# Kernel optimization log

Hardware: AMD Instinct MI355X
Metric: run time of the kernel (lower is better)

## Reference

```python
import jax, jax.numpy as jnp
import numpy as np

B, N, D, H, L = 2, 1024, 256, 4, 9
HEAD = D // H  # 64
IMG_H, IMG_W = 480, 640
SINKHORN_ITERS = 20
CH = [3, 32, 64, 128, 256]


def setup_inputs() -> dict:
    key = jax.random.key(0)
    ks = iter(jax.random.split(key, 80))
    def rn(shape, s):
        return jax.random.normal(next(ks), shape, dtype=jnp.float32) * s
    inp = {}
    size = jnp.array([IMG_W, IMG_H], jnp.float32)
    inp['kpts0'] = jax.random.uniform(next(ks), (B, N, 2), dtype=jnp.float32) * size
    inp['kpts1'] = jax.random.uniform(next(ks), (B, N, 2), dtype=jnp.float32) * size
    inp['scores0'] = jax.random.uniform(next(ks), (B, N), dtype=jnp.float32)
    inp['scores1'] = jax.random.uniform(next(ks), (B, N), dtype=jnp.float32)
    inp['desc0'] = rn((B, D, N), 1.0)
    inp['desc1'] = rn((B, D, N), 1.0)
    for i in range(4):
        inp['kenc_w%d' % i] = rn((CH[i + 1], CH[i]), CH[i] ** -0.5)
        inp['kenc_b%d' % i] = rn((CH[i + 1],), 0.02)
        if i < 3:
            inp['kenc_g%d' % i] = jnp.ones((CH[i + 1],), jnp.float32)
            inp['kenc_be%d' % i] = jnp.zeros((CH[i + 1],), jnp.float32)
    s = D ** -0.5
    inp['gnn_proj_w'] = rn((L, 3, D, D), s)
    inp['gnn_proj_b'] = rn((L, 3, D), 0.02)
    inp['gnn_merge_w'] = rn((L, D, D), s)
    inp['gnn_merge_b'] = rn((L, D), 0.02)
    inp['gnn_mlp1_w'] = rn((L, 2 * D, 2 * D), (2 * D) ** -0.5)
    inp['gnn_mlp1_b'] = rn((L, 2 * D), 0.02)
    inp['gnn_ln_g'] = jnp.ones((L, 2 * D), jnp.float32)
    inp['gnn_ln_b'] = jnp.zeros((L, 2 * D), jnp.float32)
    inp['gnn_mlp2_w'] = rn((L, D, 2 * D), (2 * D) ** -0.5)
    inp['gnn_mlp2_b'] = jnp.zeros((L, D), jnp.float32)
    inp['final_w'] = rn((D, D), s)
    inp['final_b'] = rn((D,), 0.02)
    inp['bin_score'] = jnp.array(1.0, jnp.float32)
    return inp


def _conv1(x, w, b):
    # 1x1 Conv1d == per-position matmul: x [B,C,N], w [O,C], b [O]
    return jnp.einsum('oc,bcn->bon', w, x) + b[None, :, None]


def _layernorm(x, g, b, eps=1e-6):
    # matches source LayerNorm: normalize over channel dim (-2), std with ddof=1, eps added to std
    mean = jnp.mean(x, axis=1, keepdims=True)
    std = jnp.std(x, axis=1, keepdims=True, ddof=1)
    return g[None, :, None] * (x - mean) / (std + eps) + b[None, :, None]


def _normalize_kpts(kpts):
    size = jnp.array([IMG_W, IMG_H], jnp.float32)
    center = size / 2.0
    scaling = jnp.max(size) * 0.7
    return (kpts - center) / scaling


def _attn(x, src, pw, pb, mw, mb):
    # pw [3,D,D]; view(B, head_dim, n_heads, N) matches torch .view on [B,D,N]
    q = _conv1(x, pw[0], pb[0]).reshape(B, HEAD, H, -1)
    k = _conv1(src, pw[1], pb[1]).reshape(B, HEAD, H, -1)
    v = _conv1(src, pw[2], pb[2]).reshape(B, HEAD, H, -1)
    scores = jnp.einsum('bdhn,bdhm->bhnm', q, k) / (HEAD ** 0.5)
    prob = jax.nn.softmax(scores, axis=-1)
    msg = jnp.einsum('bhnm,bdhm->bdhn', prob, v).reshape(B, D, -1)
    return _conv1(msg, mw, mb)


def _sinkhorn(Z, log_mu, log_nu, iters):
    def step(uv, _):
        u, v = uv
        u = log_mu - jax.scipy.special.logsumexp(Z + v[:, None, :], axis=2)
        v = log_nu - jax.scipy.special.logsumexp(Z + u[:, :, None], axis=1)
        return (u, v), None
    init = (jnp.zeros_like(log_mu), jnp.zeros_like(log_nu))
    (u, v), _ = jax.lax.scan(step, init, None, length=iters)
    return Z + u[:, :, None] + v[:, None, :]


def _log_ot(scores, alpha, iters):
    b, m, n = scores.shape
    bins0 = jnp.broadcast_to(alpha, (b, m, 1))
    bins1 = jnp.broadcast_to(alpha, (b, 1, n))
    a = jnp.broadcast_to(alpha, (b, 1, 1))
    couplings = jnp.concatenate([jnp.concatenate([scores, bins0], -1),
                                 jnp.concatenate([bins1, a], -1)], 1)
    norm = jnp.asarray(-np.log(float(m + n)), jnp.float32)
    log_mu = jnp.concatenate([jnp.full((m,), norm, jnp.float32),
                              jnp.array([np.log(float(n))], jnp.float32) + norm])
    log_nu = jnp.concatenate([jnp.full((n,), norm, jnp.float32),
                              jnp.array([np.log(float(m))], jnp.float32) + norm])
    log_mu = jnp.broadcast_to(log_mu, (b, m + 1))
    log_nu = jnp.broadcast_to(log_nu, (b, n + 1))
    Z = _sinkhorn(couplings, log_mu, log_nu, iters)
    return Z - norm


def _superglue_fwd(kpts0, kpts1, scores0, scores1, desc0, desc1,
                   kenc_w0, kenc_b0, kenc_g0, kenc_be0,
                   kenc_w1, kenc_b1, kenc_g1, kenc_be1,
                   kenc_w2, kenc_b2, kenc_g2, kenc_be2,
                   kenc_w3, kenc_b3,
                   gnn_proj_w, gnn_proj_b, gnn_merge_w, gnn_merge_b,
                   gnn_mlp1_w, gnn_mlp1_b, gnn_ln_g, gnn_ln_b,
                   gnn_mlp2_w, gnn_mlp2_b, final_w, final_b, bin_score):
    kenc = [(kenc_w0, kenc_b0, kenc_g0, kenc_be0),
            (kenc_w1, kenc_b1, kenc_g1, kenc_be1),
            (kenc_w2, kenc_b2, kenc_g2, kenc_be2),
            (kenc_w3, kenc_b3, None, None)]

    def encode(kpts, sc):
        x = jnp.concatenate([_normalize_kpts(kpts).transpose(0, 2, 1), sc[:, None, :]], 1)  # [B,3,N]
        for (w, b, g, be) in kenc:
            x = _conv1(x, w, b)
            if g is not None:
                x = jax.nn.relu(_layernorm(x, g, be))
        return x

    desc0 = desc0 + encode(kpts0, scores0)
    desc1 = desc1 + encode(kpts1, scores1)

    # only 'cross' GNN layers execute in this fork ('self' layers are skipped via continue)
    for i in range(L):
        def prop(x, src):
            msg = _attn(x, src, gnn_proj_w[i], gnn_proj_b[i], gnn_merge_w[i], gnn_merge_b[i])
            y = jnp.concatenate([x, msg], 1)  # [B,2D,N]
            y = jax.nn.relu(_layernorm(_conv1(y, gnn_mlp1_w[i], gnn_mlp1_b[i]), gnn_ln_g[i], gnn_ln_b[i]))
            return _conv1(y, gnn_mlp2_w[i], gnn_mlp2_b[i])
        d0 = prop(desc0, desc1)
        d1 = prop(desc1, desc0)
        desc0, desc1 = desc0 + d0, desc1 + d1

    mdesc0 = _conv1(desc0, final_w, final_b)
    mdesc1 = _conv1(desc1, final_w, final_b)
    sc = jnp.einsum('bdn,bdm->bnm', mdesc0, mdesc1) / (D ** 0.5)
    return _log_ot(sc, bin_score, SINKHORN_ITERS)  # [B, N+1, N+1] log assignment matrix


def reference(kpts0, kpts1, scores0, scores1, desc0, desc1,
              kenc_w0, kenc_b0, kenc_g0, kenc_be0,
              kenc_w1, kenc_b1, kenc_g1, kenc_be1,
              kenc_w2, kenc_b2, kenc_g2, kenc_be2,
              kenc_w3, kenc_b3,
              gnn_proj_w, gnn_proj_b, gnn_merge_w, gnn_merge_b,
              gnn_mlp1_w, gnn_mlp1_b, gnn_ln_g, gnn_ln_b,
              gnn_mlp2_w, gnn_mlp2_b, final_w, final_b, bin_score):
    return _superglue_fwd(kpts0, kpts1, scores0, scores1, desc0, desc1,
                          kenc_w0, kenc_b0, kenc_g0, kenc_be0,
                          kenc_w1, kenc_b1, kenc_g1, kenc_be1,
                          kenc_w2, kenc_b2, kenc_g2, kenc_be2,
                          kenc_w3, kenc_b3,
                          gnn_proj_w, gnn_proj_b, gnn_merge_w, gnn_merge_b,
                          gnn_mlp1_w, gnn_mlp1_b, gnn_ln_g, gnn_ln_b,
                          gnn_mlp2_w, gnn_mlp2_b, final_w, final_b, bin_score)
```

## Files before the change

### kernel.cpp

```cpp
#include <hip/hip_runtime.h>
#include <hip/hip_bf16.h>
#include <math.h>

#define DEVI static __device__ __forceinline__

namespace {
constexpr int Bc   = 2;
constexpr int Nc   = 1024;
constexpr int Dc   = 256;
constexpr int NP1c = 1025;
constexpr int LDZ  = 1028;
constexpr int LDV  = 1028;
constexpr float LN_EPS = 1e-6f;
constexpr float NORMV  = -7.6246189861593985f;
constexpr float LOGNV  =  6.9314718055994531f;
}

typedef __attribute__((ext_vector_type(8))) short bf16x8;
typedef __attribute__((ext_vector_type(4))) float f32x4;

DEVI void split2(float v, __hip_bfloat16& h, __hip_bfloat16& l) {
    h = __float2bfloat16(v);
    l = __float2bfloat16(v - __bfloat162float(h));
}

#define GLDS16(gp, lp) __builtin_amdgcn_global_load_lds( \
    (const __attribute__((address_space(1))) void*)(gp), \
    (__attribute__((address_space(3))) void*)(lp), 16, 0, 0)

DEVI float block_sum_256(float v, float* scratch) {
    int t = threadIdx.x;
    scratch[t] = v;
    __syncthreads();
    for (int s = 128; s > 0; s >>= 1) {
        if (t < s) scratch[t] += scratch[t + s];
        __syncthreads();
    }
    float r = scratch[0];
    __syncthreads();
    return r;
}

DEVI void ln_relu_inplace(float* x, const float* g, const float* be, int C, float* scratch) {
    int t = threadIdx.x;
    float v = (t < C) ? x[t] : 0.f;
    float mean = block_sum_256(v, scratch) / (float)C;
    float dv = (t < C) ? (x[t] - mean) : 0.f;
    float var = block_sum_256(dv * dv, scratch) / (float)(C - 1);
    float rstd = 1.f / (sqrtf(var) + LN_EPS);
    if (t < C) x[t] = fmaxf(g[t] * dv * rstd + be[t], 0.f);
    __syncthreads();
}

__global__ __launch_bounds__(256) void kenc_kernel(
    const float* __restrict__ kpts, const float* __restrict__ scr,
    const float* __restrict__ desc_in, float* __restrict__ desc_out,
    __hip_bfloat16* __restrict__ catHi, __hip_bfloat16* __restrict__ catLo,
    const float* __restrict__ w0, const float* __restrict__ b0,
    const float* __restrict__ g0, const float* __restrict__ be0,
    const float* __restrict__ w1T, const float* __restrict__ b1,
    const float* __restrict__ g1, const float* __restrict__ be1,
    const float* __restrict__ w2T, const float* __restrict__ b2,
    const float* __restrict__ g2, const float* __restrict__ be2,
    const float* __restrict__ w3T, const float* __restrict__ b3)
{
    __shared__ float xa[256], xb[256], scratch[256];
    const int n = blockIdx.x, b = blockIdx.y, t = threadIdx.x;
    if (t == 0) {
        float kx = kpts[((long)b * Nc + n) * 2 + 0];
        float ky = kpts[((long)b * Nc + n) * 2 + 1];
        xa[0] = (kx - 320.f) * (1.f / 448.f);
        xa[1] = (ky - 240.f) * (1.f / 448.f);
        xa[2] = scr[b * Nc + n];
    }
    __syncthreads();
    if (t < 32) { float a = b0[t]; for (int c = 0; c < 3;  ++c) a += w0[t*3 + c] * xa[c]; xb[t] = a; }
    __syncthreads();
    ln_relu_inplace(xb, g0, be0, 32, scratch);
    if (t < 64) {
        float a = b1[t];
        #pragma unroll 8
        for (int c = 0; c < 32;  ++c) a += w1T[c*64 + t] * xb[c];
        xa[t] = a;
    }
    __syncthreads();
    ln_relu_inplace(xa, g1, be1, 64, scratch);
    if (t < 128) {
        float a = b2[t];
        #pragma unroll 8
        for (int c = 0; c < 64;  ++c) a += w2T[c*128 + t] * xa[c];
        xb[t] = a;
    }
    __syncthreads();
    ln_relu_inplace(xb, g2, be2, 128, scratch);
    {   float a = b3[t];
        #pragma unroll 8
        for (int c = 0; c < 128; ++c) a += w3T[c*256 + t] * xb[c];
        float v = desc_in[((long)b * Dc + t) * Nc + n] + a;
        desc_out[((long)b * Nc + n) * Dc + t] = v;
        __hip_bfloat16 h, l; split2(v, h, l);
        long cr = ((long)b * Nc + n) * 512 + t;
        catHi[cr] = h; catLo[cr] = l;
    }
}

__global__ __launch_bounds__(256) void transposeW(
    const float* __restrict__ src, float* __restrict__ dst, int O, int C)
{
    long i = (long)blockIdx.x * 256 + threadIdx.x;
    if (i >= (long)O * C) return;
    int o = (int)(i / C), c = (int)(i % C);
    dst[(long)c * O + o] = src[i];
}

template<int BM, int BN, int EPI, int BLO, int ALO>
__global__ __launch_bounds__(256) void mfma_nt(
    const short* __restrict__ Ahi0, const short* __restrict__ Alo0, int lda,
    const short* __restrict__ Bhi0, const short* __restrict__ Blo0, int ldb,
    int K, float scale, const float* __restrict__ bias,
    float* __restrict__ outF, __hip_bfloat16* __restrict__ outHi,
    __hip_bfloat16* __restrict__ outLo,
    __hip_bfloat16* __restrict__ outHi2, __hip_bfloat16* __restrict__ outHi3,
    int ldo,
    long aS1, long bS1, long oS1)
{
    constexpr int MI = BM / 32;
    constexpr int NI = BN / 32;
    constexpr int instA = BM / 16, instB = BN / 16;
    constexpr int OFF_AH = 0;
    constexpr int OFF_AL = BM * 32;
    constexpr int OFF_BH = (1 + ALO) * BM * 32;
    constexpr int OFF_BL = OFF_BH + BN * 32;
    constexpr int CHUNK = ((1 + ALO) * BM + (1 + BLO) * BN) * 32;
    __shared__ short smem[2 * CHUNK];

    const int z = blockIdx.z;
    const long aOff = z * aS1, bOff = z * bS1, oOff = z * oS1;
    const short* Ah = Ahi0 + aOff;
    const short* Al = ALO ? (Alo0 + aOff) : nullptr;
    const short* Bh = Bhi0 + bOff;
    const short* Bl = BLO ? (Blo0 + bOff) : nullptr;

    const int m0 = blockIdx.y * BM, n0 = blockIdx.x * BN;
    const int t = threadIdx.x, lane = t & 63, wid = t >> 6;
    const int lr = lane & 15, lg = lane >> 4;
    const int wr = wid >> 1, wc = wid & 1;

    f32x4 acc[MI][NI];
    for (int mi = 0; mi < MI; ++mi)
        for (int ni = 0; ni < NI; ++ni)
            acc[mi][ni] = f32x4{0.f, 0.f, 0.f, 0.f};

    for (int k0 = 0; k0 < K; k0 += 64) {
        constexpr int total = (1 + ALO) * instA + (1 + BLO) * instB;
        for (int q = wid; q < total; q += 4) {
            const short* gsrc; int ldg, mi, ploff, row0;
            if (q < instA)                      { gsrc = Ah; ldg = lda; mi = q;          ploff = OFF_AH; row0 = m0; }
            else if (ALO && q < 2 * instA)      { gsrc = Al; ldg = lda; mi = q - instA;  ploff = OFF_AL; row0 = m0; }
            else {
                int rb = q - (1 + ALO) * instA;
                if (rb < instB) { gsrc = Bh; mi = rb;         ploff = OFF_BH; }
                else            { gsrc = Bl; mi = rb - instB; ploff = OFF_BL; }
                ldg = ldb; row0 = n0;
            }
            const short* g = gsrc + (long)(row0 + mi * 16 + lr) * ldg + (k0 + lg * 8);
            GLDS16(g,      smem + ploff + mi * 512);
            GLDS16(g + 32, smem + CHUNK + ploff + mi * 512);
        }
        __syncthreads();
        #pragma unroll
        for (int kc2 = 0; kc2 < 2; ++kc2) {
            const short* sm2 = smem + kc2 * CHUNK;
            bf16x8 ah[MI], al[MI];
            #pragma unroll
            for (int mi = 0; mi < MI; ++mi) {
                ah[mi] = *(const bf16x8*)(sm2 + OFF_AH + ((wr * MI + mi) * 64 + lane) * 8);
                if (ALO) al[mi] = *(const bf16x8*)(sm2 + OFF_AL + ((wr * MI + mi) * 64 + lane) * 8);
            }
            #pragma unroll
            for (int ni = 0; ni < NI; ++ni) {
                bf16x8 bh = *(const bf16x8*)(sm2 + OFF_BH + ((wc * NI + ni) * 64 + lane) * 8);
                #pragma unroll
                for (int mi = 0; mi < MI; ++mi) {
                    acc[mi][ni] = __builtin_amdgcn_mfma_f32_16x16x32_bf16(ah[mi], bh, acc[mi][ni], 0, 0, 0);
                    if (ALO) acc[mi][ni] = __builtin_amdgcn_mfma_f32_16x16x32_bf16(al[mi], bh, acc[mi][ni], 0, 0, 0);
                }
                if (BLO) {
                    bf16x8 bl = *(const bf16x8*)(sm2 + OFF_BL + ((wc * NI + ni) * 64 + lane) * 8);
                    #pragma unroll
                    for (int mi = 0; mi < MI; ++mi)
                        acc[mi][ni] = __builtin_amdgcn_mfma_f32_16x16x32_bf16(ah[mi], bl, acc[mi][ni], 0, 0, 0);
                }
            }
        }
        __syncthreads();
    }

    for (int mi = 0; mi < MI; ++mi) {
        for (int i = 0; i < 4; ++i) {
            int row = m0 + wr * (BM / 2) + mi * 16 + lg * 4 + i;
            for (int ni = 0; ni < NI; ++ni) {
                int col = n0 + wc * (BN / 2) + ni * 16 + lr;
                float v = acc[mi][ni][i] * scale;
                if (bias) v += bias[col];
                if (EPI == 0) {
                    outF[(long)row * ldo + col + oOff] = v;
                } else if (EPI == 1) {
                    __hip_bfloat16 h, l;
                    split2(v, h, l);
                    outHi[(long)row * ldo + col + oOff] = h;
                    outLo[(long)row * ldo + col + oOff] = l;
                } else if (EPI == 2) {
                    int dirb = row >> 10, rloc = row & 1023;
                    int tq = col >> 8, within = col & 255;
                    int h4 = within >> 6, hd = within & 63;
                    __hip_bfloat16 hh = __float2bfloat16(v);
                    if (tq == 2) {
                        int w2 = rloc >> 8, mloc = rloc & 255;
                        int lane2 = ((mloc & 31) >> 3) * 16 + (hd & 15);
                        long idx = ((((long)(dirb*4+h4)*4 + w2)*8 + (mloc>>5))*4 + (hd>>4))*512 + lane2*8 + (mloc&7);
                        outHi2[idx] = hh;
                    } else {
                        int lane2 = ((hd & 31) >> 3) * 16 + (rloc & 15);
                        long idx = (((long)(dirb*4+h4)*64 + (rloc>>4))*2 + (hd>>5))*512 + lane2*8 + (hd&7);
                        if (tq == 0) outHi[idx] = hh;
                        else         outHi3[idx] = hh;
                    }
                } else {
                    long i256 = (long)row * 256 + col;
                    v += outF[i256];
                    outF[i256] = v;
                    __hip_bfloat16 h, l;
                    split2(v, h, l);
                    outHi[(long)row * 512 + col] = h;
                    outLo[(long)row * 512 + col] = l;
                }
            }
        }
    }
}

__global__ __launch_bounds__(256) void attn_fused(
    const __hip_bfloat16* __restrict__ qFh,
    const __hip_bfloat16* __restrict__ kFh, const __hip_bfloat16* __restrict__ vFh,
    __hip_bfloat16* __restrict__ catHi)
{
    __shared__ short pLds[4 * 16 * 256];
    __shared__ float redm[4][16], reds[4][16];
    const int y = blockIdx.y;
    const int dir = y >> 3, b = (y >> 2) & 1, h = y & 3;
    const int q0 = blockIdx.x * 16;
    const int t = threadIdx.x, lane = t & 63, w = t >> 6;
    const int lr = lane & 15, lg = lane >> 4;
    const int dbQ = dir * 2 + b;
    const int srcdb = (1 - dir) * 2 + b;
    const short* qh = (const short*)qFh;
    const short* kh = (const short*)kFh;
    const short* vh = (const short*)vFh;

    const long qbase = (((long)(dbQ * 4 + h)) * 64 + (q0 >> 4)) * 2;
    bf16x8 ah[2];
    #pragma unroll
    for (int kc = 0; kc < 2; ++kc)
        ah[kc] = *(const bf16x8*)(qh + (qbase + kc) * 512 + lane * 8);

    f32x4 acc[16];
    #pragma unroll
    for (int ni = 0; ni < 16; ++ni) acc[ni] = f32x4{0.f, 0.f, 0.f, 0.f};

    const long kbase0 = (((long)(srcdb * 4 + h)) * 64 + w * 16) * 2;
    #pragma unroll
    for (int ni = 0; ni < 16; ++ni) {
        long kb = (kbase0 + ni * 2) * 512 + lane * 8;
        bf16x8 bh0 = *(const bf16x8*)(kh + kb);
        bf16x8 bh1 = *(const bf16x8*)(kh + kb + 512);
        acc[ni] = __builtin_amdgcn_mfma_f32_16x16x32_bf16(ah[0], bh0, acc[ni], 0, 0, 0);
        acc[ni] = __builtin_amdgcn_mfma_f32_16x16x32_bf16(ah[1], bh1, acc[ni], 0, 0, 0);
    }

    float mx[4] = {-1e30f, -1e30f, -1e30f, -1e30f};
    #pragma unroll
    for (int ni = 0; ni < 16; ++ni)
        #pragma unroll
        for (int i = 0; i < 4; ++i) {
            float v = acc[ni][i] * 0.125f;
            acc[ni][i] = v;
            mx[i] = fmaxf(mx[i], v);
        }
    #pragma unroll
    for (int off = 1; off < 16; off <<= 1)
        #pragma unroll
        for (int i = 0; i < 4; ++i) mx[i] = fmaxf(mx[i], __shfl_xor(mx[i], off));
    if (lr == 0)
        #pragma unroll
        for (int i = 0; i < 4; ++i) redm[w][lg * 4 + i] = mx[i];
    __syncthreads();
    float Mv[4];
    #pragma unroll
    for (int i = 0; i < 4; ++i)
        Mv[i] = fmaxf(fmaxf(redm[0][lg*4+i], redm[1][lg*4+i]),
                      fmaxf(redm[2][lg*4+i], redm[3][lg*4+i]));
    float sm[4] = {0.f, 0.f, 0.f, 0.f};
    #pragma unroll
    for (int ni = 0; ni < 16; ++ni)
        #pragma unroll
        for (int i = 0; i < 4; ++i) {
            float e = __expf(acc[ni][i] - Mv[i]);
            acc[ni][i] = e;
            sm[i] += e;
        }
    #pragma unroll
    for (int off = 1; off < 16; off <<= 1)
        #pragma unroll
        for (int i = 0; i < 4; ++i) sm[i] += __shfl_xor(sm[i], off);
    if (lr == 0)
        #pragma unroll
        for (int i = 0; i < 4; ++i) reds[w][lg * 4 + i] = sm[i];
    __syncthreads();
    float inv[4];
    #pragma unroll
    for (int i = 0; i < 4; ++i)
        inv[i] = 1.f / (reds[0][lg*4+i] + reds[1][lg*4+i] + reds[2][lg*4+i] + reds[3][lg*4+i]);

    char* pB = (char*)pLds + w * 8192;
    #pragma unroll
    for (int ni = 0; ni < 16; ++ni)
        #pragma unroll
        for (int i = 0; i < 4; ++i) {
            int q = lg * 4 + i, m = ni * 16 + lr;
            int byte = (q * 512 + m * 2) ^ ((q & 7) << 4);
            *(short*)(pB + byte) = (short)__bfloat16_as_ushort(__float2bfloat16(acc[ni][i] * inv[i]));
        }
    __syncthreads();

    f32x4 acc2[4];
    #pragma unroll
    for (int bi = 0; bi < 4; ++bi) acc2[bi] = f32x4{0.f, 0.f, 0.f, 0.f};
    const long vbase0 = (((long)(srcdb * 4 + h)) * 4 + w) * 8;
    #pragma unroll
    for (int km = 0; km < 8; ++km) {
        int rb = (lr * 512 + km * 64 + lg * 16) ^ ((lr & 7) << 4);
        bf16x8 pa = *(const bf16x8*)(pB + rb);
        #pragma unroll
        for (int bi = 0; bi < 4; ++bi) {
            long vr = ((vbase0 + km) * 4 + bi) * 512 + lane * 8;
            bf16x8 vhf = *(const bf16x8*)(vh + vr);
            acc2[bi] = __builtin_amdgcn_mfma_f32_16x16x32_bf16(pa, vhf, acc2[bi], 0, 0, 0);
        }
    }
    __syncthreads();
    float* pr = (float*)pLds;
    #pragma unroll
    for (int bi = 0; bi < 4; ++bi)
        #pragma unroll
        for (int i = 0; i < 4; ++i)
            pr[w * 1024 + (lg * 4 + i) * 64 + bi * 16 + lr] = acc2[bi][i];
    __syncthreads();
    #pragma unroll
    for (int k = 0; k < 4; ++k) {
        int e = t + k * 256;
        float v = pr[e] + pr[1024 + e] + pr[2048 + e] + pr[3072 + e];
        int q = e >> 6, d = e & 63;
        long a = ((long)dbQ * 1024 + q0 + q) * 512 + 256 + h * 64 + d;
        catHi[a] = __float2bfloat16(v);
    }
}

__global__ __launch_bounds__(256) void ln_relu_w(
    const float* __restrict__ y, const float* __restrict__ g, const float* __restrict__ be,
    __hip_bfloat16* __restrict__ hi)
{
    const int t = threadIdx.x, lane = t & 63, w = t >> 6;
    const long row = (long)blockIdx.x * 4 + w;
    const float* src = y + row * 512;
    float4 v0 = ((const float4*)src)[lane * 2];
    float4 v1 = ((const float4*)src)[lane * 2 + 1];
    float s = v0.x + v0.y + v0.z + v0.w + v1.x + v1.y + v1.z + v1.w;
    float q = v0.x*v0.x + v0.y*v0.y + v0.z*v0.z + v0.w*v0.w
            + v1.x*v1.x + v1.y*v1.y + v1.z*v1.z + v1.w*v1.w;
    #pragma unroll
    for (int off = 1; off < 64; off <<= 1) {
        s += __shfl_xor(s, off);
        q += __shfl_xor(q, off);
    }
    float mean = s / 512.f;
    float var = fmaxf((q - 512.f * mean * mean) / 511.f, 0.f);
    float rstd = 1.f / (sqrtf(var) + LN_EPS);
    float4 g0 = ((const float4*)g)[lane * 2], g1 = ((const float4*)g)[lane * 2 + 1];
    float4 b0 = ((const float4*)be)[lane * 2], b1 = ((const float4*)be)[lane * 2 + 1];
    float xv[8] = {v0.x, v0.y, v0.z, v0.w, v1.x, v1.y, v1.z, v1.w};
    float gv[8] = {g0.x, g0.y, g0.z, g0.w, g1.x, g1.y, g1.z, g1.w};
    float bv[8] = {b0.x, b0.y, b0.z, b0.w, b1.x, b1.y, b1.z, b1.w};
    bf16x8 outv;
    #pragma unroll
    for (int k = 0; k < 8; ++k) {
        float o = fmaxf(gv[k] * (xv[k] - mean) * rstd + bv[k], 0.f);
        outv[k] = (short)__bfloat16_as_ushort(__float2bfloat16(o));
    }
    *(bf16x8*)((short*)hi + row * 512 + lane * 8) = outv;
}

__global__ __launch_bounds__(256) void wconv_plain(
    const float* __restrict__ w, __hip_bfloat16* __restrict__ hi, __hip_bfloat16* __restrict__ lo, long total)
{
    long i = (long)blockIdx.x * 256 + threadIdx.x;
    if (i >= total) return;
    __hip_bfloat16 h, l; split2(w[i], h, l);
    hi[i] = h; lo[i] = l;
}

__global__ __launch_bounds__(256) void wconv_proj(
    const float* __restrict__ w, __hip_bfloat16* __restrict__ hi, __hip_bfloat16* __restrict__ lo)
{
    long i = (long)blockIdx.x * 256 + threadIdx.x;
    if (i >= 9L * 768 * 256) return;
    long l9 = i / (768 * 256);
    int rem = (int)(i % (768 * 256));
    int op = rem / 256, c = rem % 256;
    int tq = op / 256, within = op % 256;
    int h = within / 64, hd = within % 64;
    int o = tq * 256 + hd * 4 + h;
    float v = w[(l9 * 768 + o) * 256 + c];
    __hip_bfloat16 hh, ll; split2(v, hh, ll);
    hi[i] = hh; lo[i] = ll;
}

__global__ void wconv_proj_bias(const float* __restrict__ b, float* __restrict__ bp)
{
    int i = blockIdx.x * 256 + threadIdx.x;
    if (i >= 9 * 768) return;
    int l9 = i / 768, op = i % 768;
    int tq = op / 256, within = op % 256;
    int h = within / 64, hd = within % 64;
    bp[i] = b[(l9 * 3 + tq) * 256 + hd * 4 + h];
}

__global__ __launch_bounds__(256) void wconv_mergeT(
    const float* __restrict__ w, __hip_bfloat16* __restrict__ hi, __hip_bfloat16* __restrict__ lo)
{
    long i = (long)blockIdx.x * 256 + threadIdx.x;
    if (i >= 9L * 256 * 256) return;
    long l9 = i / (256 * 256);
    int rem = (int)(i % (256 * 256));
    int c = rem / 256, j = rem % 256;
    int h = c / 64, hd = c % 64;
    float v = w[(l9 * 256 + j) * 256 + (hd * 4 + h)];
    __hip_bfloat16 hh, ll; split2(v, hh, ll);
    hi[i] = hh; lo[i] = ll;
}

__global__ __launch_bounds__(256) void wconv_m1(
    const float* __restrict__ w,
    __hip_bfloat16* __restrict__ m1cHi, __hip_bfloat16* __restrict__ m1cLo,
    __hip_bfloat16* __restrict__ m1bHi, __hip_bfloat16* __restrict__ m1bLo)
{
    long i = (long)blockIdx.x * 256 + threadIdx.x;
    if (i >= 9L * 512 * 512) return;
    long lo9 = i / 512;
    int c = (int)(i % 512);
    __hip_bfloat16 hh, ll; split2(w[i], hh, ll);
    if (c < 256) { m1cHi[lo9 * 512 + c] = hh; m1cLo[lo9 * 512 + c] = ll; }
    else         { m1bHi[lo9 * 256 + c - 256] = hh; m1bLo[lo9 * 256 + c - 256] = ll; }
}

__global__ __launch_bounds__(64) void bias_fold(
    const float* __restrict__ w1, const float* __restrict__ b1,
    const float* __restrict__ bm, float* __restrict__ out)
{
    int og = blockIdx.x;
    int l = og >> 9, o = og & 511;
    int t = threadIdx.x;
    float s = 0.f;
    for (int j = t; j < 256; j += 64)
        s += w1[((long)l * 512 + o) * 512 + 256 + j] * bm[l * 256 + j];
    for (int off = 32; off > 0; off >>= 1) s += __shfl_down(s, off);
    if (t == 0) out[og] = b1[(long)l * 512 + o] + s;
}

__global__ void bins_fill(float* __restrict__ Z, const float* __restrict__ alpha_p)
{
    float alpha = alpha_p[0];
    int idx = blockIdx.x * 256 + threadIdx.x;
    int b = blockIdx.y;
    float* Zb = Z + (long)b * NP1c * LDZ;
    if (idx < NP1c) Zb[(long)1024 * LDZ + idx] = alpha;
    else { int i = idx - NP1c; if (i < 1024) Zb[(long)i * LDZ + 1024] = alpha; }
}

__global__ void transpose_np1(const float* __restrict__ Z, float* __restrict__ ZT)
{
    __shared__ float tile[32][33];
    int b = blockIdx.z;
    int i0 = blockIdx.y * 32, j0 = blockIdx.x * 32;
    int tx = threadIdx.x, ty = threadIdx.y;
    const float* Zb = Z + (long)b * NP1c * LDZ;
    float* Tb = ZT + (long)b * NP1c * LDZ;
    for (int ii = ty; ii < 32; ii += 8) {
        int i = i0 + ii, j = j0 + tx;
        if (i < NP1c && j < NP1c) tile[ii][tx] = Zb[(long)i * LDZ + j];
    }
    __syncthreads();
    for (int jj = ty; jj < 32; jj += 8) {
        int j = j0 + jj, i = i0 + tx;
        if (j < NP1c && i < NP1c) Tb[(long)j * LDZ + i] = tile[tx][jj];
    }
}

__global__ void zero_vec(float* __restrict__ v, int n)
{
    int i = blockIdx.x * 256 + threadIdx.x;
    if (i < n) v[i] = 0.f;
}

__global__ __launch_bounds__(256) void sinkhorn_lse(
    const float* __restrict__ M, const float* __restrict__ addv, float* __restrict__ outv)
{
    const int t = threadIdx.x, lane = t & 63, w = t >> 6;
    long rowid = (long)blockIdx.x * 4 + w;
    if (rowid >= 2 * NP1c) return;
    int b = rowid >= NP1c ? 1 : 0;
    int i = (int)(rowid - (long)b * NP1c);
    const float* row = M + ((long)b * NP1c + i) * LDZ;
    const float* av = addv + (long)b * LDV;
    float m = -1e30f, s = 0.f;
    #pragma unroll
    for (int k = 0; k < 4; ++k) {
        float4 x = ((const float4*)row)[lane * 4 + k];
        float4 a = ((const float4*)av)[lane * 4 + k];
        float u0 = x.x + a.x, u1 = x.y + a.y, u2 = x.z + a.z, u3 = x.w + a.w;
        float mk = fmaxf(fmaxf(u0, u1), fmaxf(u2, u3));
        float sk = __expf(u0 - mk) + __expf(u1 - mk) + __expf(u2 - mk) + __expf(u3 - mk);
        if (mk > m) { s = s * __expf(m - mk) + sk; m = mk; }
        else        { s += sk * __expf(mk - m); }
    }
    if (lane == 0) {
        float v4 = row[1024] + av[1024];
        if (v4 > m) { s = s * __expf(m - v4) + 1.f; m = v4; }
        else        { s += __expf(v4 - m); }
    }
    #pragma unroll
    for (int off = 1; off < 64; off <<= 1) {
        float m2 = __shfl_xor(m, off);
        float s2 = __shfl_xor(s, off);
        float mm = fmaxf(m, m2);
        s = s * __expf(m - mm) + s2 * __expf(m2 - mm);
        m = mm;
    }
    if (lane == 0) {
        float lse = m + __logf(s);
        float lmu = (i < 1024) ? NORMV : (LOGNV + NORMV);
        outv[(long)b * LDV + i] = lmu - lse;
    }
}

__global__ __launch_bounds__(256) void final_out_k(
    const float* __restrict__ Z, const float* __restrict__ u,
    const float* __restrict__ v, float* __restrict__ outp)
{
    const int i = blockIdx.x, b = blockIdx.y, t = threadIdx.x;
    const float* row = Z + ((long)b * NP1c + i) * LDZ;
    float* orow = outp + ((long)b * NP1c + i) * NP1c;
    float ui = u[(long)b * LDV + i];
    for (int j = t; j < NP1c; j += 256)
        orow[j] = row[j] + ui + v[(long)b * LDV + j] - NORMV;
}

extern "C" void kernel_launch(void* const* d_in, const int* in_sizes, int n_in,
                              void* d_out, int out_size, void* d_ws, size_t ws_size,
                              hipStream_t stream)
{
    (void)in_sizes; (void)n_in; (void)out_size; (void)ws_size;
    const float* kpts0   = (const float*)d_in[0];
    const float* kpts1   = (const float*)d_in[1];
    const float* scores0 = (const float*)d_in[2];
    const float* scores1 = (const float*)d_in[3];
    const float* desc0   = (const float*)d_in[4];
    const float* desc1   = (const float*)d_in[5];
    const float* kw0 = (const float*)d_in[6];  const float* kb0 = (const float*)d_in[7];
    const float* kg0 = (const float*)d_in[8];  const float* ke0 = (const float*)d_in[9];
    const float* kw1 = (const float*)d_in[10]; const float* kb1 = (const float*)d_in[11];
    const float* kg1 = (const float*)d_in[12]; const float* ke1 = (const float*)d_in[13];
    const float* kw2 = (const float*)d_in[14]; const float* kb2 = (const float*)d_in[15];
    const float* kg2 = (const float*)d_in[16]; const float* ke2 = (const float*)d_in[17];
    const float* kw3 = (const float*)d_in[18]; const float* kb3 = (const float*)d_in[19];
    const float* gnn_proj_w  = (const float*)d_in[20];
    const float* gnn_proj_b  = (const float*)d_in[21];
    const float* gnn_merge_w = (const float*)d_in[22];
    const float* gnn_merge_b = (const float*)d_in[23];
    const float* gnn_mlp1_w  = (const float*)d_in[24];
    const float* gnn_mlp1_b  = (const float*)d_in[25];
    const float* gnn_ln_g    = (const float*)d_in[26];
    const float* gnn_ln_b    = (const float*)d_in[27];
    const float* gnn_mlp2_w  = (const float*)d_in[28];
    const float* gnn_mlp2_b  = (const float*)d_in[29];
    const float* final_w     = (const float*)d_in[30];
    const float* final_b     = (const float*)d_in[31];
    const float* bin_score   = (const float*)d_in[32];

    char* wsb = (char*)d_ws;
    size_t off = 0;
    auto alloc = [&](size_t bytes) -> void* {
        void* p = wsb + off;
        off = (off + bytes + 255) & ~(size_t)255;
        return p;
    };
    typedef __hip_bfloat16 bf;
    const long ROWS = 4L * Nc;
    float* descF  = (float*)alloc(ROWS * 256 * 4);
    float* ybufF  = (float*)alloc(ROWS * 512 * 4);
    float* Zm     = (float*)alloc((long)Bc * NP1c * LDZ * 4);
    float* ZT     = (float*)alloc((long)Bc * NP1c * LDZ * 4);
    float* uvec   = (float*)alloc(Bc * LDV * 4);
    float* vvec   = (float*)alloc(Bc * LDV * 4);
    float* projBp = (float*)alloc(9L * 768 * 4);
    float* b1c    = (float*)alloc(9L * 512 * 4);
    float* kw1T   = (float*)alloc(32L * 64 * 4);
    float* kw2T   = (float*)alloc(64L * 128 * 4);
    float* kw3T   = (float*)alloc(128L * 256 * 4);
    bf* catHi = (bf*)alloc(ROWS * 512 * 2);  bf* catLo = (bf*)alloc(ROWS * 512 * 2);
    bf* qFh = (bf*)alloc(1048576 * 2);
    bf* kFh = (bf*)alloc(1048576 * 2);
    bf* vFh = (bf*)alloc(1048576 * 2);
    bf* ybHi  = (bf*)alloc(ROWS * 512 * 2);
    bf* mdHi  = (bf*)alloc(ROWS * 256 * 2);  bf* mdLo  = (bf*)alloc(ROWS * 256 * 2);
    bf* projHi = (bf*)alloc(9L*768*256*2);   bf* projLo = (bf*)alloc(9L*768*256*2);
    bf* mrgTHi = (bf*)alloc(9L*256*256*2);   bf* mrgTLo = (bf*)alloc(9L*256*256*2);
    bf* m1bHi  = (bf*)alloc(9L*512*256*2);   bf* m1bLo  = (bf*)alloc(9L*512*256*2);
    bf* m1cHi  = (bf*)alloc(9L*512*512*2);   bf* m1cLo  = (bf*)alloc(9L*512*512*2);
    bf* m2Hi   = (bf*)alloc(9L*256*512*2);   bf* m2Lo   = (bf*)alloc(9L*256*512*2);
    bf* finHi  = (bf*)alloc(256L*256*2);     bf* finLo  = (bf*)alloc(256L*256*2);

    wconv_proj<<<dim3((9*768*256+255)/256), 256, 0, stream>>>(gnn_proj_w, projHi, projLo);
    wconv_proj_bias<<<dim3(27), 256, 0, stream>>>(gnn_proj_b, projBp);
    wconv_mergeT<<<dim3((9*256*256+255)/256), 256, 0, stream>>>(gnn_merge_w, mrgTHi, mrgTLo);
    wconv_m1<<<dim3((int)((9L*512*512+255)/256)), 256, 0, stream>>>(gnn_mlp1_w, m1cHi, m1cLo, m1bHi, m1bLo);
    wconv_plain<<<dim3((9*256*512+255)/256), 256, 0, stream>>>(gnn_mlp2_w, m2Hi, m2Lo, 9L*256*512);
    wconv_plain<<<dim3((256*256+255)/256), 256, 0, stream>>>(final_w, finHi, finLo, 256L*256);
    bias_fold<<<dim3(9*512), 64, 0, stream>>>(gnn_mlp1_w, gnn_mlp1_b, gnn_merge_b, b1c);
    transposeW<<<dim3((64*32+255)/256), 256, 0, stream>>>(kw1, kw1T, 64, 32);
    transposeW<<<dim3((128*64+255)/256), 256, 0, stream>>>(kw2, kw2T, 128, 64);
    transposeW<<<dim3((256*128+255)/256), 256, 0, stream>>>(kw3, kw3T, 256, 128);
    mfma_nt<128,128,1,1,1><<<dim3(2,4,9), 256, 0, stream>>>(
        (const short*)m1bHi, (const short*)m1bLo, 256,
        (const short*)mrgTHi, (const short*)mrgTLo, 256,
        256, 1.f, nullptr,
        nullptr, m1cHi + 256, m1cLo + 256, nullptr, nullptr, 512,
        512L*256, 256L*256, 512L*512);

    kenc_kernel<<<dim3(Nc, Bc), 256, 0, stream>>>(kpts0, scores0, desc0, descF,
        catHi, catLo,
        kw0, kb0, kg0, ke0, kw1T, kb1, kg1, ke1, kw2T, kb2, kg2, ke2, kw3T, kb3);
    kenc_kernel<<<dim3(Nc, Bc), 256, 0, stream>>>(kpts1, scores1, desc1, descF + 2L*Nc*256,
        catHi + 2L*Nc*512, catLo + 2L*Nc*512,
        kw0, kb0, kg0, ke0, kw1T, kb1, kg1, ke1, kw2T, kb2, kg2, ke2, kw3T, kb3);

    for (int l = 0; l < 9; ++l) {
        mfma_nt<64,64,2,0,0><<<dim3(12,64,1), 256, 0, stream>>>(
            (const short*)catHi, nullptr, 512,
            (const short*)(projHi + (long)l*768*256), nullptr, 256,
            256, 1.f, projBp + (long)l*768,
            nullptr, qFh, nullptr, vFh, kFh, 0,
            0, 0, 0);
        attn_fused<<<dim3(64, 16), 256, 0, stream>>>(qFh, kFh, vFh, catHi);
        mfma_nt<64,64,0,0,0><<<dim3(8,64,1), 256, 0, stream>>>(
            (const short*)catHi, nullptr, 512,
            (const short*)(m1cHi + (long)l*512*512), nullptr, 512,
            512, 1.f, b1c + (long)l*512,
            ybufF, nullptr, nullptr, nullptr, nullptr, 512,
            0, 0, 0);
        ln_relu_w<<<dim3(1024), 256, 0, stream>>>(
            ybufF, gnn_ln_g + (long)l*512, gnn_ln_b + (long)l*512, ybHi);
        mfma_nt<64,64,3,0,0><<<dim3(4,64,1), 256, 0, stream>>>(
            (const short*)ybHi, nullptr, 512,
            (const short*)(m2Hi + (long)l*256*512), nullptr, 512,
            512, 1.f, gnn_mlp2_b + (long)l*256,
            descF, catHi, catLo, nullptr, nullptr, 0,
            0, 0, 0);
    }

    mfma_nt<64,64,1,0,1><<<dim3(4,64,1), 256, 0, stream>>>(
        (const short*)catHi, (const short*)catLo, 512,
        (const short*)finHi, nullptr, 256,
        256, 1.f, final_b,
        nullptr, mdHi, mdLo, nullptr, nullptr, 256,
        0, 0, 0);
    mfma_nt<64,64,0,1,1><<<dim3(16,16,2), 256, 0, stream>>>(
        (const short*)mdHi, (const short*)mdLo, 256,
        (const short*)mdHi + 2048L*256, (const short*)mdLo + 2048L*256, 256,
        256, 1.f/16.f, nullptr,
        Zm, nullptr, nullptr, nullptr, nullptr, LDZ,
        1024L*256, 1024L*256, (long)NP1c*LDZ);
    bins_fill<<<dim3(9,2), 256, 0, stream>>>(Zm, bin_score);

    transpose_np1<<<dim3(33,33,2), dim3(32,8), 0, stream>>>(Zm, ZT);
    zero_vec<<<dim3((2*LDV+255)/256), 256, 0, stream>>>(vvec, Bc * LDV);
    zero_vec<<<dim3((2*LDV+255)/256), 256, 0, stream>>>(uvec, Bc * LDV);
    for (int it = 0; it < 20; ++it) {
        sinkhorn_lse<<<dim3(513), 256, 0, stream>>>(Zm, vvec, uvec);
        sinkhorn_lse<<<dim3(513), 256, 0, stream>>>(ZT, uvec, vvec);
    }
    final_out_k<<<dim3(NP1c, Bc), 256, 0, stream>>>(Zm, uvec, vvec, (float*)d_out);
}
```

Measured before the change: 907.4 us.

## Merge kenc launches, write MLP1 output as bf16, deepen GEMM K-chunk

Merges the two keypoint-encoder launches into one grid and the two zero-fill launches into one, cutting launch count. The MLP1 GEMM now writes a bf16 intermediate in place of fp32, and LayerNorm reads and overwrites that bf16 buffer, halving that round-trip traffic and dropping the fp32 scratch buffer. The GEMM template gains a K-chunk count parameter, set to 4 for most GEMMs, so each sync stage loads 128 K elements, at the cost of more LDS per block. Rounding the pre-LayerNorm activations to bf16 adds some numerical error.

```diff
diff --git a/kernel.cpp b/kernel.cpp
--- a/kernel.cpp
+++ b/kernel.cpp
@@ -24,6 +24,8 @@
     l = __float2bfloat16(v - __bfloat162float(h));
 }
 
+DEVI float bf2f(short u) { return __uint_as_float(((unsigned)(unsigned short)u) << 16); }
+
 #define GLDS16(gp, lp) __builtin_amdgcn_global_load_lds( \
     (const __attribute__((address_space(1))) void*)(gp), \
     (__attribute__((address_space(3))) void*)(lp), 16, 0, 0)
@@ -53,8 +55,10 @@
 }
 
 __global__ __launch_bounds__(256) void kenc_kernel(
-    const float* __restrict__ kpts, const float* __restrict__ scr,
-    const float* __restrict__ desc_in, float* __restrict__ desc_out,
+    const float* __restrict__ kpts0, const float* __restrict__ kpts1,
+    const float* __restrict__ scr0, const float* __restrict__ scr1,
+    const float* __restrict__ desc0, const float* __restrict__ desc1,
+    float* __restrict__ descF,
     __hip_bfloat16* __restrict__ catHi, __hip_bfloat16* __restrict__ catLo,
     const float* __restrict__ w0, const float* __restrict__ b0,
     const float* __restrict__ g0, const float* __restrict__ be0,
@@ -65,7 +69,11 @@
     const float* __restrict__ w3T, const float* __restrict__ b3)
 {
     __shared__ float xa[256], xb[256], scratch[256];
-    const int n = blockIdx.x, b = blockIdx.y, t = threadIdx.x;
+    const int n = blockIdx.x, db = blockIdx.y, t = threadIdx.x;
+    const int dir = db >> 1, b = db & 1;
+    const float* kpts = dir ? kpts1 : kpts0;
+    const float* scr  = dir ? scr1  : scr0;
+    const float* dsc  = dir ? desc1 : desc0;
     if (t == 0) {
         float kx = kpts[((long)b * Nc + n) * 2 + 0];
         float ky = kpts[((long)b * Nc + n) * 2 + 1];
@@ -96,10 +104,10 @@
     {   float a = b3[t];
         #pragma unroll 8
         for (int c = 0; c < 128; ++c) a += w3T[c*256 + t] * xb[c];
-        float v = desc_in[((long)b * Dc + t) * Nc + n] + a;
-        desc_out[((long)b * Nc + n) * Dc + t] = v;
+        float v = dsc[((long)b * Dc + t) * Nc + n] + a;
+        descF[((long)db * Nc + n) * Dc + t] = v;
         __hip_bfloat16 h, l; split2(v, h, l);
-        long cr = ((long)b * Nc + n) * 512 + t;
+        long cr = ((long)db * Nc + n) * 512 + t;
         catHi[cr] = h; catLo[cr] = l;
     }
 }
@@ -113,7 +121,7 @@
     dst[(long)c * O + o] = src[i];
 }
 
-template<int BM, int BN, int EPI, int BLO, int ALO>
+template<int BM, int BN, int EPI, int BLO, int ALO, int BKC>
 __global__ __launch_bounds__(256) void mfma_nt(
     const short* __restrict__ Ahi0, const short* __restrict__ Alo0, int lda,
     const short* __restrict__ Bhi0, const short* __restrict__ Blo0, int ldb,
@@ -132,7 +140,7 @@
     constexpr int OFF_BH = (1 + ALO) * BM * 32;
     constexpr int OFF_BL = OFF_BH + BN * 32;
     constexpr int CHUNK = ((1 + ALO) * BM + (1 + BLO) * BN) * 32;
-    __shared__ short smem[2 * CHUNK];
+    __shared__ short smem[BKC * CHUNK];
 
     const int z = blockIdx.z;
     const long aOff = z * aS1, bOff = z * bS1, oOff = z * oS1;
@@ -151,7 +159,7 @@
         for (int ni = 0; ni < NI; ++ni)
             acc[mi][ni] = f32x4{0.f, 0.f, 0.f, 0.f};
 
-    for (int k0 = 0; k0 < K; k0 += 64) {
+    for (int k0 = 0; k0 < K; k0 += 32 * BKC) {
         constexpr int total = (1 + ALO) * instA + (1 + BLO) * instB;
         for (int q = wid; q < total; q += 4) {
             const short* gsrc; int ldg, mi, ploff, row0;
@@ -164,12 +172,13 @@
                 ldg = ldb; row0 = n0;
             }
             const short* g = gsrc + (long)(row0 + mi * 16 + lr) * ldg + (k0 + lg * 8);
-            GLDS16(g,      smem + ploff + mi * 512);
-            GLDS16(g + 32, smem + CHUNK + ploff + mi * 512);
+            #pragma unroll
+            for (int c = 0; c < BKC; ++c)
+                GLDS16(g + 32 * c, smem + c * CHUNK + ploff + mi * 512);
         }
         __syncthreads();
         #pragma unroll
-        for (int kc2 = 0; kc2 < 2; ++kc2) {
+        for (int kc2 = 0; kc2 < BKC; ++kc2) {
             const short* sm2 = smem + kc2 * CHUNK;
             bf16x8 ah[MI], al[MI];
             #pragma unroll
@@ -226,7 +235,7 @@
                         if (tq == 0) outHi[idx] = hh;
                         else         outHi3[idx] = hh;
                     }
-                } else {
+                } else if (EPI == 3) {
                     long i256 = (long)row * 256 + col;
                     v += outF[i256];
                     outF[i256] = v;
@@ -234,6 +243,8 @@
                     split2(v, h, l);
                     outHi[(long)row * 512 + col] = h;
                     outLo[(long)row * 512 + col] = l;
+                } else {
+                    outHi[(long)row * ldo + col + oOff] = __float2bfloat16(v);
                 }
             }
         }
@@ -367,17 +378,18 @@
 }
 
 __global__ __launch_bounds__(256) void ln_relu_w(
-    const float* __restrict__ y, const float* __restrict__ g, const float* __restrict__ be,
-    __hip_bfloat16* __restrict__ hi)
+    __hip_bfloat16* __restrict__ y, const float* __restrict__ g, const float* __restrict__ be)
 {
     const int t = threadIdx.x, lane = t & 63, w = t >> 6;
     const long row = (long)blockIdx.x * 4 + w;
-    const float* src = y + row * 512;
-    float4 v0 = ((const float4*)src)[lane * 2];
-    float4 v1 = ((const float4*)src)[lane * 2 + 1];
-    float s = v0.x + v0.y + v0.z + v0.w + v1.x + v1.y + v1.z + v1.w;
-    float q = v0.x*v0.x + v0.y*v0.y + v0.z*v0.z + v0.w*v0.w
-            + v1.x*v1.x + v1.y*v1.y + v1.z*v1.z + v1.w*v1.w;
+    short* src = (short*)y + row * 512;
+    bf16x8 r = *(const bf16x8*)(src + lane * 8);
+    float xv[8];
+    #pragma unroll
+    for (int k = 0; k < 8; ++k) xv[k] = bf2f(r[k]);
+    float s = 0.f, q = 0.f;
+    #pragma unroll
+    for (int k = 0; k < 8; ++k) { s += xv[k]; q += xv[k] * xv[k]; }
     #pragma unroll
     for (int off = 1; off < 64; off <<= 1) {
         s += __shfl_xor(s, off);
@@ -388,7 +400,6 @@
     float rstd = 1.f / (sqrtf(var) + LN_EPS);
     float4 g0 = ((const float4*)g)[lane * 2], g1 = ((const float4*)g)[lane * 2 + 1];
     float4 b0 = ((const float4*)be)[lane * 2], b1 = ((const float4*)be)[lane * 2 + 1];
-    float xv[8] = {v0.x, v0.y, v0.z, v0.w, v1.x, v1.y, v1.z, v1.w};
     float gv[8] = {g0.x, g0.y, g0.z, g0.w, g1.x, g1.y, g1.z, g1.w};
     float bv[8] = {b0.x, b0.y, b0.z, b0.w, b1.x, b1.y, b1.z, b1.w};
     bf16x8 outv;
@@ -397,7 +408,7 @@
         float o = fmaxf(gv[k] * (xv[k] - mean) * rstd + bv[k], 0.f);
         outv[k] = (short)__bfloat16_as_ushort(__float2bfloat16(o));
     }
-    *(bf16x8*)((short*)hi + row * 512 + lane * 8) = outv;
+    *(bf16x8*)(src + lane * 8) = outv;
 }
 
 __global__ __launch_bounds__(256) void wconv_plain(
@@ -506,10 +517,10 @@
     }
 }
 
-__global__ void zero_vec(float* __restrict__ v, int n)
+__global__ void zero_vec2(float* __restrict__ a, float* __restrict__ b, int n)
 {
     int i = blockIdx.x * 256 + threadIdx.x;
-    if (i < n) v[i] = 0.f;
+    if (i < n) { a[i] = 0.f; b[i] = 0.f; }
 }
 
 __global__ __launch_bounds__(256) void sinkhorn_lse(
@@ -607,7 +618,6 @@
     typedef __hip_bfloat16 bf;
     const long ROWS = 4L * Nc;
     float* descF  = (float*)alloc(ROWS * 256 * 4);
-    float* ybufF  = (float*)alloc(ROWS * 512 * 4);
     float* Zm     = (float*)alloc((long)Bc * NP1c * LDZ * 4);
     float* ZT     = (float*)alloc((long)Bc * NP1c * LDZ * 4);
     float* uvec   = (float*)alloc(Bc * LDV * 4);
@@ -640,37 +650,34 @@
     transposeW<<<dim3((64*32+255)/256), 256, 0, stream>>>(kw1, kw1T, 64, 32);
     transposeW<<<dim3((128*64+255)/256), 256, 0, stream>>>(kw2, kw2T, 128, 64);
     transposeW<<<dim3((256*128+255)/256), 256, 0, stream>>>(kw3, kw3T, 256, 128);
-    mfma_nt<128,128,1,1,1><<<dim3(2,4,9), 256, 0, stream>>>(
+    mfma_nt<128,128,1,1,1,2><<<dim3(2,4,9), 256, 0, stream>>>(
         (const short*)m1bHi, (const short*)m1bLo, 256,
         (const short*)mrgTHi, (const short*)mrgTLo, 256,
         256, 1.f, nullptr,
         nullptr, m1cHi + 256, m1cLo + 256, nullptr, nullptr, 512,
         512L*256, 256L*256, 512L*512);
 
-    kenc_kernel<<<dim3(Nc, Bc), 256, 0, stream>>>(kpts0, scores0, desc0, descF,
-        catHi, catLo,
+    kenc_kernel<<<dim3(Nc, 4), 256, 0, stream>>>(
+        kpts0, kpts1, scores0, scores1, desc0, desc1, descF, catHi, catLo,
         kw0, kb0, kg0, ke0, kw1T, kb1, kg1, ke1, kw2T, kb2, kg2, ke2, kw3T, kb3);
-    kenc_kernel<<<dim3(Nc, Bc), 256, 0, stream>>>(kpts1, scores1, desc1, descF + 2L*Nc*256,
-        catHi + 2L*Nc*512, catLo + 2L*Nc*512,
-        kw0, kb0, kg0, ke0, kw1T, kb1, kg1, ke1, kw2T, kb2, kg2, ke2, kw3T, kb3);
 
     for (int l = 0; l < 9; ++l) {
-        mfma_nt<64,64,2,0,0><<<dim3(12,64,1), 256, 0, stream>>>(
+        mfma_nt<64,64,2,0,0,4><<<dim3(12,64,1), 256, 0, stream>>>(
             (const short*)catHi, nullptr, 512,
             (const short*)(projHi + (long)l*768*256), nullptr, 256,
             256, 1.f, projBp + (long)l*768,
             nullptr, qFh, nullptr, vFh, kFh, 0,
             0, 0, 0);
         attn_fused<<<dim3(64, 16), 256, 0, stream>>>(qFh, kFh, vFh, catHi);
-        mfma_nt<64,64,0,0,0><<<dim3(8,64,1), 256, 0, stream>>>(
+        mfma_nt<64,64,4,0,0,4><<<dim3(8,64,1), 256, 0, stream>>>(
             (const short*)catHi, nullptr, 512,
             (const short*)(m1cHi + (long)l*512*512), nullptr, 512,
             512, 1.f, b1c + (long)l*512,
-            ybufF, nullptr, nullptr, nullptr, nullptr, 512,
+            nullptr, ybHi, nullptr, nullptr, nullptr, 512,
             0, 0, 0);
         ln_relu_w<<<dim3(1024), 256, 0, stream>>>(
-            ybufF, gnn_ln_g + (long)l*512, gnn_ln_b + (long)l*512, ybHi);
-        mfma_nt<64,64,3,0,0><<<dim3(4,64,1), 256, 0, stream>>>(
+            ybHi, gnn_ln_g + (long)l*512, gnn_ln_b + (long)l*512);
+        mfma_nt<64,64,3,0,0,4><<<dim3(4,64,1), 256, 0, stream>>>(
             (const short*)ybHi, nullptr, 512,
             (const short*)(m2Hi + (long)l*256*512), nullptr, 512,
             512, 1.f, gnn_mlp2_b + (long)l*256,
@@ -678,13 +685,13 @@
             0, 0, 0);
     }
 
-    mfma_nt<64,64,1,0,1><<<dim3(4,64,1), 256, 0, stream>>>(
+    mfma_nt<64,64,1,0,1,4><<<dim3(4,64,1), 256, 0, stream>>>(
         (const short*)catHi, (const short*)catLo, 512,
         (const short*)finHi, nullptr, 256,
         256, 1.f, final_b,
         nullptr, mdHi, mdLo, nullptr, nullptr, 256,
         0, 0, 0);
-    mfma_nt<64,64,0,1,1><<<dim3(16,16,2), 256, 0, stream>>>(
+    mfma_nt<64,64,0,1,1,2><<<dim3(16,16,2), 256, 0, stream>>>(
         (const short*)mdHi, (const short*)mdLo, 256,
         (const short*)mdHi + 2048L*256, (const short*)mdLo + 2048L*256, 256,
         256, 1.f/16.f, nullptr,
@@ -693,8 +700,7 @@
     bins_fill<<<dim3(9,2), 256, 0, stream>>>(Zm, bin_score);
 
     transpose_np1<<<dim3(33,33,2), dim3(32,8), 0, stream>>>(Zm, ZT);
-    zero_vec<<<dim3((2*LDV+255)/256), 256, 0, stream>>>(vvec, Bc * LDV);
-    zero_vec<<<dim3((2*LDV+255)/256), 256, 0, stream>>>(uvec, Bc * LDV);
+    zero_vec2<<<dim3((2*LDV+255)/256), 256, 0, stream>>>(uvec, vvec, Bc * LDV);
     for (int it = 0; it < 20; ++it) {
         sinkhorn_lse<<<dim3(513), 256, 0, stream>>>(Zm, vvec, uvec);
         sinkhorn_lse<<<dim3(513), 256, 0, stream>>>(ZT, uvec, vvec);
```

After: 879.4 us. -3.1%, faster.
